# Optimization experiments

Measured on AMD Instinct MI355X. Metric: run time of the kernel, lower is better.

Reference implementation:

```python
import jax, jax.numpy as jnp
import numpy as np

D_MODEL, N_HEADS, D_STATE, N_GROUPS, CHUNK = 2048, 32, 64, 1, 256
BATCH, SEQLEN = 2, 4096


def setup_inputs() -> dict:
    key = jax.random.key(0)
    ks = jax.random.split(key, 8)
    s = 0.02
    d, h, n, g = D_MODEL, N_HEADS, D_STATE, N_GROUPS
    return {
        "x": jax.random.normal(ks[0], (BATCH, SEQLEN, d), jnp.float32),
        "A_log": jnp.log(jnp.arange(1, h + 1, dtype=jnp.float32)),
        "D": jnp.ones((h,), jnp.float32),
        "B_w": jax.random.normal(ks[1], (g * n, d), jnp.float32) * s,
        "B_b": jnp.zeros((g * n,), jnp.float32),
        "C_w": jax.random.normal(ks[2], (g * n, d), jnp.float32) * s,
        "C_b": jnp.zeros((g * n,), jnp.float32),
        "dt_w": jax.random.normal(ks[3], (h, d), jnp.float32) * s,
        "dt_b": jnp.zeros((h,), jnp.float32),
        "out_w": jax.random.normal(ks[4], (d, d), jnp.float32) * s,
        "out_b": jnp.zeros((d,), jnp.float32),
    }


def segsum(v):
    # v: [..., T] -> [..., T, T]; out[i,j] = sum_{k=j+1..i} v[k] for i>=j, -inf else
    cs = jnp.cumsum(v, axis=-1)
    seg = cs[..., :, None] - cs[..., None, :]
    T = v.shape[-1]
    mask = jnp.tril(jnp.ones((T, T), bool))
    return jnp.where(mask, seg, -jnp.inf)


def _ssd(x, A_log, D, B_w, B_b, C_w, C_b, dt_w, dt_b, out_w, out_b):
    b, t, d = x.shape
    h = A_log.shape[0]
    n = B_w.shape[0] // N_GROUPS
    p = d // h
    l = CHUNK
    c = t // l

    A = -jnp.exp(A_log.astype(jnp.float32))                      # [h]
    B = (x @ B_w.T + B_b).reshape(b, t, N_GROUPS, n)             # g=1
    C = (x @ C_w.T + C_b).reshape(b, t, N_GROUPS, n)
    B = jnp.broadcast_to(B, (b, t, h, n))                        # repeat groups -> heads
    C = jnp.broadcast_to(C, (b, t, h, n))
    dt = jax.nn.softplus(x @ dt_w.T + dt_b)                      # [b,t,h]
    xh = x.reshape(b, t, h, p)

    # chunked SSD (Mamba2 mamba_chunk_scan_combined math)
    xc = xh.reshape(b, c, l, h, p)
    Bc = B.reshape(b, c, l, h, n)
    Cc = C.reshape(b, c, l, h, n)
    dtc = dt.reshape(b, c, l, h)
    dA = jnp.transpose(dtc * A, (0, 3, 1, 2))                    # [b,h,c,l]
    A_cumsum = jnp.cumsum(dA, axis=-1)                           # [b,h,c,l]

    # 1. intra-chunk (diagonal blocks)
    L = jnp.exp(segsum(dA))                                      # [b,h,c,l,l]
    xdt = xc * dtc[..., None]                                    # [b,c,l,h,p]
    Y_diag = jnp.einsum('bclhn,bcshn,bhcls,bcshp->bclhp', Cc, Bc, L, xdt)

    # 2. per-chunk final states
    decay_states = jnp.exp(A_cumsum[..., -1:] - A_cumsum)        # [b,h,c,l]
    states = jnp.einsum('bclhn,bhcl,bclhp->bchpn', Bc, decay_states, xdt)

    # 3. inter-chunk recurrence on chunk states
    states = jnp.concatenate([jnp.zeros_like(states[:, :1]), states], axis=1)  # [b,c+1,h,p,n]
    dA_last = jnp.pad(A_cumsum[..., -1], ((0, 0), (0, 0), (1, 0)))             # [b,h,c+1]
    decay_chunk = jnp.exp(segsum(dA_last))                                     # [b,h,c+1,c+1]
    new_states = jnp.einsum('bhzc,bchpn->bzhpn', decay_chunk, states)
    prev_states = new_states[:, :-1]                                           # [b,c,h,p,n]

    # 4. state -> output contribution
    state_decay_out = jnp.exp(A_cumsum)                          # [b,h,c,l]
    Y_off = jnp.einsum('bclhn,bchpn,bhcl->bclhp', Cc, prev_states, state_decay_out)

    Y = (Y_diag + Y_off).reshape(b, t, h, p) + D[None, None, :, None] * xh
    return Y.reshape(b, t, d) @ out_w.T + out_b


def reference(x, A_log, D, B_w, B_b, C_w, C_b, dt_w, dt_b, out_w, out_b):
    return _ssd(x, A_log, D, B_w, B_b, C_w, C_b, dt_w, dt_b, out_w, out_b)
```

## Files before the change

### kernel.cpp

```cpp
#include <hip/hip_runtime.h>
#include <hip/hip_bf16.h>
#include <math.h>

namespace {
constexpr int kDModel = 2048;
constexpr int kHeads  = 32;
constexpr int kState  = 64;
constexpr int kP      = 64;
constexpr int kChunk  = 256;
constexpr int kNChunk = 16;
constexpr int kBatch  = 2;
constexpr int kSeq    = 4096;
constexpr int kM      = kBatch * kSeq;
}

typedef __bf16 bf16_t;
typedef __attribute__((ext_vector_type(8))) __bf16 bf16x8;
typedef __attribute__((ext_vector_type(4))) __bf16 bf16x4;
typedef __attribute__((ext_vector_type(4))) float f32x4;

__device__ __forceinline__ void gload_lds16(const void* g, void* l) {
    __builtin_amdgcn_global_load_lds(
        (const __attribute__((address_space(1))) void*)g,
        (__attribute__((address_space(3))) void*)l,
        16, 0, 0);
}

__global__ __launch_bounds__(256)
void gemm_bcdt(const bf16_t* __restrict__ A, const bf16_t* __restrict__ W,
               const float* __restrict__ b0, const float* __restrict__ b1,
               const float* __restrict__ b2,
               bf16_t* __restrict__ o0h, bf16_t* __restrict__ o1h,
               float* __restrict__ o2f)
{
    constexpr int K = kDModel;
    __shared__ __bf16 AstS[64 * 32];
    __shared__ __bf16 WstS[128 * 32];
    const int tid  = threadIdx.x;
    const int lane = tid & 63;
    const int wave = tid >> 6;
    const int wm = (wave >> 1) * 32;
    const int wn = (wave & 1) * 64;
    const int l15 = lane & 15, quad = lane >> 4;
    const int m0 = blockIdx.y * 64;
    const int n0 = blockIdx.x * 128;
    const int u0 = tid, u1 = tid + 256;

    f32x4 acc[2][4];
    #pragma unroll
    for (int i = 0; i < 2; ++i)
        #pragma unroll
        for (int j = 0; j < 4; ++j)
            acc[i][j] = (f32x4){0.f, 0.f, 0.f, 0.f};

    for (int k0 = 0; k0 < K; k0 += 32) {
        gload_lds16(A + (size_t)(m0 + (tid >> 2)) * K + k0 + (tid & 3) * 8, AstS + tid * 8);
        gload_lds16(W + (size_t)(n0 + (u0 >> 2)) * K + k0 + (u0 & 3) * 8, WstS + u0 * 8);
        gload_lds16(W + (size_t)(n0 + (u1 >> 2)) * K + k0 + (u1 & 3) * 8, WstS + u1 * 8);
        __syncthreads();
        bf16x8 af[2], bfr[4];
        #pragma unroll
        for (int mi = 0; mi < 2; ++mi)
            af[mi] = *reinterpret_cast<const bf16x8*>(&AstS[(wm + mi * 16 + l15) * 32 + quad * 8]);
        #pragma unroll
        for (int ni = 0; ni < 4; ++ni)
            bfr[ni] = *reinterpret_cast<const bf16x8*>(&WstS[(wn + ni * 16 + l15) * 32 + quad * 8]);
        #pragma unroll
        for (int mi = 0; mi < 2; ++mi)
            #pragma unroll
            for (int ni = 0; ni < 4; ++ni)
                acc[mi][ni] = __builtin_amdgcn_mfma_f32_16x16x32_bf16(
                    af[mi], bfr[ni], acc[mi][ni], 0, 0, 0);
        __syncthreads();
    }

    #pragma unroll
    for (int mi = 0; mi < 2; ++mi) {
        #pragma unroll
        for (int reg = 0; reg < 4; ++reg) {
            const int r = m0 + wm + mi * 16 + quad * 4 + reg;
            #pragma unroll
            for (int ni = 0; ni < 4; ++ni) {
                const float v = acc[mi][ni][reg];
                const int n = n0 + wn + ni * 16 + l15;
                if (n < 64) {
                    o0h[(size_t)r * 64 + n] = (bf16_t)(v + b0[n]);
                } else if (n < 128) {
                    o1h[(size_t)r * 64 + (n - 64)] = (bf16_t)(v + b1[n - 64]);
                } else if (n < 160) {
                    float z = v + b2[n - 128];
                    o2f[(size_t)r * 32 + (n - 128)] = (z > 20.f) ? z : log1pf(expf(z));
                }
            }
        }
    }
}

__global__ __launch_bounds__(512, 2)
void gemm256_out(const bf16_t* __restrict__ Ap, const bf16_t* __restrict__ Bp,
                 const float* __restrict__ bias, float* __restrict__ C)
{
    constexpr int M = 8192, N = 2048, NT = 2048 / 32;
    __shared__ __bf16 Ab[3][4 * 256 * 8];
    __shared__ __bf16 Bb[3][4 * 256 * 8];
    const int tid  = threadIdx.x;
    const int lane = tid & 63;
    const int wave = tid >> 6;
    const int l15 = lane & 15, quad = lane >> 4;
    const int bid = blockIdx.x;
    const int mt = (bid & 7) * 4 + ((bid >> 3) & 3);
    const int nt = bid >> 5;
    const int m0 = mt * 256;
    const int n0 = nt * 256;
    const int wm = (wave >> 2) * 128;
    const int wn = (wave & 3) * 64;

    const int u0 = tid, u1 = tid + 512;
    auto stage = [&](int t2, int stb) {
        const int ks0 = t2 * 4;
        const bf16_t* As = Ap + ((size_t)ks0 * M + m0) * 8;
        const bf16_t* Bs = Bp + ((size_t)ks0 * N + n0) * 8;
        __bf16* Al = &Ab[stb][0];
        __bf16* Bl = &Bb[stb][0];
        gload_lds16(As + ((size_t)(u0 >> 8) * M + (u0 & 255)) * 8, Al + u0 * 8);
        gload_lds16(As + ((size_t)(u1 >> 8) * M + (u1 & 255)) * 8, Al + u1 * 8);
        gload_lds16(Bs + ((size_t)(u0 >> 8) * N + (u0 & 255)) * 8, Bl + u0 * 8);
        gload_lds16(Bs + ((size_t)(u1 >> 8) * N + (u1 & 255)) * 8, Bl + u1 * 8);
    };

    f32x4 acc[8][4];
    #pragma unroll
    for (int i = 0; i < 8; ++i)
        #pragma unroll
        for (int j = 0; j < 4; ++j)
            acc[i][j] = (f32x4){0.f, 0.f, 0.f, 0.f};

    stage(0, 0);
    stage(1, 1);
    asm volatile("s_waitcnt vmcnt(4)" ::: "memory");
    __builtin_amdgcn_s_barrier();

    int cur = 0;
    for (int t = 0; t < NT; ++t) {
        const __bf16* Ac = &Ab[cur][0];
        const __bf16* Bc = &Bb[cur][0];
        int stb = cur + 2; if (stb >= 3) stb -= 3;

        bf16x8 af[4], bfr[4];
        #pragma unroll
        for (int mi = 0; mi < 4; ++mi)
            af[mi] = *reinterpret_cast<const bf16x8*>(
                &Ac[(quad * 256 + wm + mi * 16 + l15) * 8]);
        #pragma unroll
        for (int nj = 0; nj < 4; ++nj)
            bfr[nj] = *reinterpret_cast<const bf16x8*>(
                &Bc[(quad * 256 + wn + nj * 16 + l15) * 8]);
        if (t < NT - 2) stage(t + 2, stb);
        __builtin_amdgcn_s_setprio(1);
        #pragma unroll
        for (int mi = 0; mi < 4; ++mi)
            #pragma unroll
            for (int nj = 0; nj < 4; ++nj)
                acc[mi][nj] = __builtin_amdgcn_mfma_f32_16x16x32_bf16(
                    af[mi], bfr[nj], acc[mi][nj], 0, 0, 0);
        __builtin_amdgcn_s_setprio(0);

        #pragma unroll
        for (int mi = 0; mi < 4; ++mi)
            af[mi] = *reinterpret_cast<const bf16x8*>(
                &Ac[(quad * 256 + wm + 64 + mi * 16 + l15) * 8]);
        __builtin_amdgcn_s_setprio(1);
        #pragma unroll
        for (int mi = 0; mi < 4; ++mi)
            #pragma unroll
            for (int nj = 0; nj < 4; ++nj)
                acc[4 + mi][nj] = __builtin_amdgcn_mfma_f32_16x16x32_bf16(
                    af[mi], bfr[nj], acc[4 + mi][nj], 0, 0, 0);
        __builtin_amdgcn_s_setprio(0);

        if (t < NT - 2) {
            asm volatile("s_waitcnt vmcnt(4)" ::: "memory");
        } else if (t < NT - 1) {
            asm volatile("s_waitcnt vmcnt(0)" ::: "memory");
        }
        if (t < NT - 1) __builtin_amdgcn_s_barrier();
        cur = cur + 1; if (cur == 3) cur = 0;
    }

    float bia[4];
    #pragma unroll
    for (int nj = 0; nj < 4; ++nj) bia[nj] = bias[n0 + wn + nj * 16 + l15];
    #pragma unroll
    for (int mi = 0; mi < 8; ++mi) {
        #pragma unroll
        for (int reg = 0; reg < 4; ++reg) {
            const int r = m0 + wm + mi * 16 + quad * 4 + reg;
            #pragma unroll
            for (int nj = 0; nj < 4; ++nj) {
                const int c = n0 + wn + nj * 16 + l15;
                C[(size_t)r * N + c] = acc[mi][nj][reg] + bia[nj];
            }
        }
    }
}

__global__ __launch_bounds__(256)
void cvt_bf16_kernel(const float* __restrict__ src, bf16_t* __restrict__ dst, int n)
{
    const int i = (blockIdx.x * 256 + threadIdx.x) * 4;
    if (i + 3 < n) {
        const float4 v = *reinterpret_cast<const float4*>(src + i);
        dst[i + 0] = (bf16_t)v.x;
        dst[i + 1] = (bf16_t)v.y;
        dst[i + 2] = (bf16_t)v.z;
        dst[i + 3] = (bf16_t)v.w;
    }
}

__global__ __launch_bounds__(256)
void pack_wob_kernel(const float* __restrict__ W, bf16_t* __restrict__ Wp)
{
    const int idx = blockIdx.x * 256 + threadIdx.x;
    const int n = idx >> 8, ks = idx & 255;
    const float4 v0 = *reinterpret_cast<const float4*>(W + (size_t)n * 2048 + ks * 8);
    const float4 v1 = *reinterpret_cast<const float4*>(W + (size_t)n * 2048 + ks * 8 + 4);
    bf16x8 o;
    o[0] = (__bf16)v0.x; o[1] = (__bf16)v0.y; o[2] = (__bf16)v0.z; o[3] = (__bf16)v0.w;
    o[4] = (__bf16)v1.x; o[5] = (__bf16)v1.y; o[6] = (__bf16)v1.z; o[7] = (__bf16)v1.w;
    *reinterpret_cast<bf16x8*>(Wp + ((size_t)ks * 2048 + n) * 8) = o;
}

__global__ __launch_bounds__(256)
void pack_w_kernel(const float* __restrict__ B_w, const float* __restrict__ C_w,
                   const float* __restrict__ dt_w, bf16_t* __restrict__ wcat)
{
    const int idx = blockIdx.x * 256 + threadIdx.x;
    const int r = idx >> 11, k = idx & 2047;
    float v = 0.f;
    if (r < 64)       v = B_w[r * 2048 + k];
    else if (r < 128) v = C_w[(r - 64) * 2048 + k];
    else if (r < 160) v = dt_w[(r - 128) * 2048 + k];
    wcat[idx] = (bf16_t)v;
}

__global__ __launch_bounds__(kChunk)
void dtcumsum_kernel(const float* __restrict__ dtm, const float* __restrict__ A_log,
                     float* __restrict__ Acs)
{
    const int blk = blockIdx.x;
    const int ci = blk & (kNChunk - 1);
    const int hi = (blk >> 4) & (kHeads - 1);
    const int bi = blk >> 9;
    const int t = threadIdx.x;
    const float Ah = -expf(A_log[hi]);
    __shared__ float s[kChunk];
    s[t] = dtm[((size_t)bi * kSeq + ci * kChunk + t) * kHeads + hi] * Ah;
    __syncthreads();
    for (int off = 1; off < kChunk; off <<= 1) {
        const float add = (t >= off) ? s[t - off] : 0.f;
        __syncthreads();
        s[t] += add;
        __syncthreads();
    }
    Acs[((size_t)(bi * kHeads + hi) * kNChunk + ci) * kChunk + t] = s[t];
}

__global__ __launch_bounds__(256)
void bT_kernel(const bf16_t* __restrict__ Bb16, bf16_t* __restrict__ bTg)
{
    const int ci = blockIdx.x & (kNChunk - 1);
    const int bi = blockIdx.x >> 4;
    const size_t rowbase = (size_t)bi * kSeq + ci * kChunk;
    __shared__ __bf16 T[64 * 264];
    const int tid = threadIdx.x;
    bf16x8 v[8];
    #pragma unroll
    for (int e = 0; e < 8; ++e)
        v[e] = *reinterpret_cast<const bf16x8*>(Bb16 + (rowbase + tid) * 64 + e * 8);
    #pragma unroll
    for (int e = 0; e < 8; ++e)
        #pragma unroll
        for (int j = 0; j < 8; ++j)
            T[(e * 8 + j) * 264 + tid] = v[e][j];
    __syncthreads();
    const int n = tid >> 2, seg = (tid & 3) * 64;
    bf16_t* dst = bTg + ((size_t)(bi * kNChunk + ci)) * (64 * 256) + n * 256 + seg;
    #pragma unroll
    for (int j = 0; j < 8; ++j) {
        *reinterpret_cast<bf16x8*>(dst + j * 8) =
            *reinterpret_cast<const bf16x8*>(&T[n * 264 + seg + j * 8]);
    }
}

__global__ __launch_bounds__(256)
void xdtT_kernel(const bf16_t* __restrict__ xb, const float* __restrict__ dtm,
                 bf16_t* __restrict__ xdtT)
{
    const int blk = blockIdx.x;
    const int hi = blk & (kHeads - 1);
    const int ci = (blk >> 5) & (kNChunk - 1);
    const int bi = blk >> 9;
    const size_t rowbase = (size_t)bi * kSeq + ci * kChunk;
    __shared__ __bf16 T[64 * 264];
    const int tid = threadIdx.x;
    const float d = dtm[(rowbase + tid) * kHeads + hi];
    bf16x8 v[8];
    #pragma unroll
    for (int e = 0; e < 8; ++e)
        v[e] = *reinterpret_cast<const bf16x8*>(xb + (rowbase + tid) * kDModel + hi * kP + e * 8);
    #pragma unroll
    for (int e = 0; e < 8; ++e)
        #pragma unroll
        for (int j = 0; j < 8; ++j)
            T[(e * 8 + j) * 264 + tid] = (__bf16)((float)v[e][j] * d);
    __syncthreads();
    const int p = tid >> 2, seg = (tid & 3) * 64;
    bf16_t* dst = xdtT + (size_t)blk * (64 * 256) + p * 256 + seg;
    #pragma unroll
    for (int j = 0; j < 8; ++j) {
        *reinterpret_cast<bf16x8*>(dst + j * 8) =
            *reinterpret_cast<const bf16x8*>(&T[p * 264 + seg + j * 8]);
    }
}

__global__ __launch_bounds__(256)
void states_mfma(const bf16_t* __restrict__ xdtT, const bf16_t* __restrict__ bTg,
                 const float* __restrict__ Acs, float* __restrict__ states)
{
    const int blk = blockIdx.x;
    const int hi = blk & (kHeads - 1);
    const int ci = (blk >> 5) & (kNChunk - 1);
    const int bi = blk >> 9;
    __shared__ __bf16 Xa[64 * 264];
    __shared__ __bf16 Bt[64 * 264];
    __shared__ float dec[kChunk];
    const int tid = threadIdx.x;
    const int lane = tid & 63;
    const int wave = tid >> 6;
    const int l15 = lane & 15, quad = lane >> 4;

    const float* acs = Acs + ((size_t)(bi * kHeads + hi) * kNChunk + ci) * kChunk;
    dec[tid] = expf(acs[kChunk - 1] - acs[tid]);
    __syncthreads();

    const bf16_t* bsrc = bTg + ((size_t)(bi * kNChunk + ci)) * (64 * 256);
    const bf16_t* xsrc = xdtT + (size_t)blk * (64 * 256);
    #pragma unroll
    for (int e = 0; e < 8; ++e) {
        const int u = e * 256 + tid;
        const int r = u >> 5, seg = (u & 31) * 8;
        *reinterpret_cast<bf16x8*>(&Bt[r * 264 + seg]) =
            *reinterpret_cast<const bf16x8*>(bsrc + r * 256 + seg);
        bf16x8 xv = *reinterpret_cast<const bf16x8*>(xsrc + r * 256 + seg);
        bf16x8 xo;
        #pragma unroll
        for (int j = 0; j < 8; ++j)
            xo[j] = (__bf16)((float)xv[j] * dec[seg + j]);
        *reinterpret_cast<bf16x8*>(&Xa[r * 264 + seg]) = xo;
    }
    __syncthreads();

    f32x4 acc[4];
    #pragma unroll
    for (int ni = 0; ni < 4; ++ni) acc[ni] = (f32x4){0.f, 0.f, 0.f, 0.f};
    #pragma unroll
    for (int kk = 0; kk < 8; ++kk) {
        const bf16x8 af = *reinterpret_cast<const bf16x8*>(
            &Xa[(wave * 16 + l15) * 264 + kk * 32 + quad * 8]);
        #pragma unroll
        for (int ni = 0; ni < 4; ++ni) {
            const bf16x8 bf = *reinterpret_cast<const bf16x8*>(
                &Bt[(ni * 16 + l15) * 264 + kk * 32 + quad * 8]);
            acc[ni] = __builtin_amdgcn_mfma_f32_16x16x32_bf16(af, bf, acc[ni], 0, 0, 0);
        }
    }
    float* sp = states + (size_t)blk * (kP * kState);
    #pragma unroll
    for (int reg = 0; reg < 4; ++reg) {
        const int p = wave * 16 + quad * 4 + reg;
        #pragma unroll
        for (int ni = 0; ni < 4; ++ni)
            sp[(size_t)p * kState + ni * 16 + l15] = acc[ni][reg];
    }
}

__global__ __launch_bounds__(256)
void chunkscan_kernel(const float* __restrict__ states, const float* __restrict__ Acs,
                      float* __restrict__ prevs)
{
    const int q  = blockIdx.x & 15;
    const int hi = (blockIdx.x >> 4) & (kHeads - 1);
    const int bi = blockIdx.x >> 9;
    const int e  = q * 256 + threadIdx.x;
    __shared__ float ea[kNChunk];
    if (threadIdx.x < kNChunk)
        ea[threadIdx.x] = expf(Acs[((size_t)(bi * kHeads + hi) * kNChunk + threadIdx.x)
                                   * kChunk + kChunk - 1]);
    __syncthreads();
    float P = 0.f;
    prevs[((size_t)(bi * kNChunk + 0) * kHeads + hi) * (kP * kState) + e] = 0.f;
    for (int c = 1; c < kNChunk; ++c) {
        P = fmaf(ea[c - 1], P,
                 states[((size_t)(bi * kNChunk + (c - 1)) * kHeads + hi) * (kP * kState) + e]);
        prevs[((size_t)(bi * kNChunk + c) * kHeads + hi) * (kP * kState) + e] = P;
    }
}

__global__ __launch_bounds__(256)
void ychunk_mfma(const float* __restrict__ x, const bf16_t* __restrict__ Bb16,
                 const bf16_t* __restrict__ Cb16, const bf16_t* __restrict__ xdtT,
                 const float* __restrict__ Acs, const float* __restrict__ prevs,
                 const float* __restrict__ Dvec, bf16_t* __restrict__ Yp)
{
    const int blk = blockIdx.x;
    const int lt = blk & 3;
    const int hi = (blk >> 2) & (kHeads - 1);
    const int ci = (blk >> 7) & (kNChunk - 1);
    const int bi = blk >> 11;
    __shared__ float acs_s[kChunk];
    __shared__ __bf16 Cs[64 * 72];
    __shared__ __bf16 Bs[64 * 72];
    __shared__ __bf16 Xt[64 * 72];
    __shared__ __bf16 Sp[64 * 72];
    const int tid = threadIdx.x;
    const int lane = tid & 63;
    const int wave = tid >> 6;
    const int l15 = lane & 15, quad = lane >> 4;
    const size_t rowbase = (size_t)bi * kSeq + ci * kChunk;
    const bf16_t* xdsrc = xdtT + ((size_t)((bi * kNChunk + ci) * kHeads + hi)) * (64 * 256);

    acs_s[tid] = Acs[((size_t)(bi * kHeads + hi) * kNChunk + ci) * kChunk + tid];
    #pragma unroll
    for (int e = 0; e < 2; ++e) {
        const int u = e * 256 + tid;
        const int r = u >> 3, seg = (u & 7) * 8;
        *reinterpret_cast<bf16x8*>(&Cs[r * 72 + seg]) =
            *reinterpret_cast<const bf16x8*>(Cb16 + (rowbase + lt * 64 + r) * 64 + seg);
    }
    const float* pp = prevs + ((size_t)(bi * kNChunk + ci) * kHeads + hi) * (kP * kState);
    #pragma unroll
    for (int e = 0; e < 4; ++e) {
        const int idx = e * 1024 + tid * 4;
        const int r = idx >> 6, c = idx & 63;
        const float4 vp = *reinterpret_cast<const float4*>(pp + idx);
        bf16x4 p4;
        p4[0] = (__bf16)vp.x; p4[1] = (__bf16)vp.y;
        p4[2] = (__bf16)vp.z; p4[3] = (__bf16)vp.w;
        *reinterpret_cast<bf16x4*>(&Bs[r * 72 + c]) = p4;
    }
    __syncthreads();

    bf16x8 af[2];
    af[0] = *reinterpret_cast<const bf16x8*>(&Cs[(wave * 16 + l15) * 72 + quad * 8]);
    af[1] = *reinterpret_cast<const bf16x8*>(&Cs[(wave * 16 + l15) * 72 + 32 + quad * 8]);

    f32x4 yacc[4];
    #pragma unroll
    for (int ni = 0; ni < 4; ++ni) yacc[ni] = (f32x4){0.f, 0.f, 0.f, 0.f};
    #pragma unroll
    for (int ni = 0; ni < 4; ++ni) {
        const bf16x8 b0 = *reinterpret_cast<const bf16x8*>(&Bs[(ni * 16 + l15) * 72 + quad * 8]);
        const bf16x8 b1 = *reinterpret_cast<const bf16x8*>(&Bs[(ni * 16 + l15) * 72 + 32 + quad * 8]);
        yacc[ni] = __builtin_amdgcn_mfma_f32_16x16x32_bf16(af[0], b0, yacc[ni], 0, 0, 0);
        yacc[ni] = __builtin_amdgcn_mfma_f32_16x16x32_bf16(af[1], b1, yacc[ni], 0, 0, 0);
    }
    const int mrow = wave * 16 + quad * 4;
    {
        float es[4];
        #pragma unroll
        for (int reg = 0; reg < 4; ++reg) es[reg] = expf(acs_s[lt * 64 + mrow + reg]);
        #pragma unroll
        for (int ni = 0; ni < 4; ++ni)
            #pragma unroll
            for (int reg = 0; reg < 4; ++reg) yacc[ni][reg] *= es[reg];
    }

    for (int st = 0; st <= lt; ++st) {
        __syncthreads();
        #pragma unroll
        for (int e = 0; e < 2; ++e) {
            const int u = e * 256 + tid;
            const int r = u >> 3, seg = (u & 7) * 8;
            *reinterpret_cast<bf16x8*>(&Bs[r * 72 + seg]) =
                *reinterpret_cast<const bf16x8*>(Bb16 + (rowbase + st * 64 + r) * 64 + seg);
            *reinterpret_cast<bf16x8*>(&Xt[r * 72 + seg]) =
                *reinterpret_cast<const bf16x8*>(xdsrc + r * 256 + st * 64 + seg);
        }
        __syncthreads();
        f32x4 sacc[4];
        #pragma unroll
        for (int ni = 0; ni < 4; ++ni) sacc[ni] = (f32x4){0.f, 0.f, 0.f, 0.f};
        #pragma unroll
        for (int ni = 0; ni < 4; ++ni) {
            const bf16x8 b0 = *reinterpret_cast<const bf16x8*>(&Bs[(ni * 16 + l15) * 72 + quad * 8]);
            const bf16x8 b1 = *reinterpret_cast<const bf16x8*>(&Bs[(ni * 16 + l15) * 72 + 32 + quad * 8]);
            sacc[ni] = __builtin_amdgcn_mfma_f32_16x16x32_bf16(af[0], b0, sacc[ni], 0, 0, 0);
            sacc[ni] = __builtin_amdgcn_mfma_f32_16x16x32_bf16(af[1], b1, sacc[ni], 0, 0, 0);
        }
        #pragma unroll
        for (int reg = 0; reg < 4; ++reg) {
            const int l = lt * 64 + mrow + reg;
            const float al = acs_s[l];
            #pragma unroll
            for (int ni = 0; ni < 4; ++ni) {
                const int scol = ni * 16 + l15;
                const int sg = st * 64 + scol;
                float v = sacc[ni][reg] * expf(al - acs_s[sg]);
                if (st == lt && sg > l) v = 0.f;
                Sp[(mrow + reg) * 72 + scol] = (__bf16)v;
            }
        }
        __syncthreads();
        const bf16x8 as0 = *reinterpret_cast<const bf16x8*>(&Sp[(wave * 16 + l15) * 72 + quad * 8]);
        const bf16x8 as1 = *reinterpret_cast<const bf16x8*>(&Sp[(wave * 16 + l15) * 72 + 32 + quad * 8]);
        #pragma unroll
        for (int ni = 0; ni < 4; ++ni) {
            const bf16x8 x0 = *reinterpret_cast<const bf16x8*>(&Xt[(ni * 16 + l15) * 72 + quad * 8]);
            const bf16x8 x1 = *reinterpret_cast<const bf16x8*>(&Xt[(ni * 16 + l15) * 72 + 32 + quad * 8]);
            yacc[ni] = __builtin_amdgcn_mfma_f32_16x16x32_bf16(as0, x0, yacc[ni], 0, 0, 0);
            yacc[ni] = __builtin_amdgcn_mfma_f32_16x16x32_bf16(as1, x1, yacc[ni], 0, 0, 0);
        }
    }

    const float Dh = Dvec[hi];
    #pragma unroll
    for (int reg = 0; reg < 4; ++reg) {
        const size_t tg = rowbase + lt * 64 + mrow + reg;
        #pragma unroll
        for (int ni = 0; ni < 4; ++ni) {
            const int p = ni * 16 + l15;
            const float v = yacc[ni][reg] + Dh * x[tg * kDModel + hi * kP + p];
            Yp[((size_t)(hi * 8 + (p >> 3)) * (size_t)kM + tg) * 8 + (p & 7)] = (bf16_t)v;
        }
    }
}

extern "C" void kernel_launch(void* const* d_in, const int* in_sizes, int n_in,
                              void* d_out, int out_size, void* d_ws, size_t ws_size,
                              hipStream_t stream)
{
    (void)in_sizes; (void)n_in; (void)out_size; (void)ws_size;
    const float* x     = (const float*)d_in[0];
    const float* A_log = (const float*)d_in[1];
    const float* Dvec  = (const float*)d_in[2];
    const float* B_w   = (const float*)d_in[3];
    const float* B_b   = (const float*)d_in[4];
    const float* C_w   = (const float*)d_in[5];
    const float* C_b   = (const float*)d_in[6];
    const float* dt_w  = (const float*)d_in[7];
    const float* dt_b  = (const float*)d_in[8];
    const float* out_w = (const float*)d_in[9];
    const float* out_b = (const float*)d_in[10];
    float* out = (float*)d_out;

    float* ws = (float*)d_ws;
    float* dtm    = ws;
    float* Acs    = dtm + (size_t)kM * kHeads;
    float* states = Acs + (size_t)kBatch * kHeads * kNChunk * kChunk;
    float* prevs  = states + (size_t)kBatch * kNChunk * kHeads * kP * kState;
    bf16_t* xb    = (bf16_t*)(prevs + (size_t)kBatch * kNChunk * kHeads * kP * kState);
    bf16_t* Y     = xb;
    bf16_t* Bb16  = xb + (size_t)kM * kDModel;
    bf16_t* Cb16  = Bb16 + (size_t)kM * kState;
    bf16_t* xdtT  = Cb16 + (size_t)kM * kState;
    bf16_t* bTg   = xdtT + (size_t)kM * kDModel;
    bf16_t* wcat  = bTg + (size_t)kBatch * kNChunk * kState * kChunk;
    bf16_t* wob   = wcat + (size_t)256 * kDModel;

    const dim3 blk(256);
    cvt_bf16_kernel<<<dim3(kM * kDModel / 1024), blk, 0, stream>>>(x, xb, kM * kDModel);
    pack_wob_kernel<<<dim3(kDModel * 256 / 256), blk, 0, stream>>>(out_w, wob);
    pack_w_kernel<<<dim3(256 * kDModel / 256), blk, 0, stream>>>(B_w, C_w, dt_w, wcat);
    gemm_bcdt<<<dim3(2, kM / 64), blk, 0, stream>>>(xb, wcat,
                                                    B_b, C_b, dt_b,
                                                    Bb16, Cb16, dtm);
    dtcumsum_kernel<<<dim3(kBatch * kHeads * kNChunk), dim3(kChunk), 0, stream>>>(dtm, A_log, Acs);
    bT_kernel<<<dim3(kBatch * kNChunk), blk, 0, stream>>>(Bb16, bTg);
    xdtT_kernel<<<dim3(kBatch * kNChunk * kHeads), blk, 0, stream>>>(xb, dtm, xdtT);
    states_mfma<<<dim3(kBatch * kNChunk * kHeads), blk, 0, stream>>>(xdtT, bTg, Acs, states);
    chunkscan_kernel<<<dim3(kBatch * kHeads * 16), blk, 0, stream>>>(states, Acs, prevs);
    ychunk_mfma<<<dim3(kBatch * kNChunk * kHeads * 4), blk, 0, stream>>>(
        x, Bb16, Cb16, xdtT, Acs, prevs, Dvec, Y);
    gemm256_out<<<dim3(256), dim3(512), 0, stream>>>(Y, wob, out_b, out);
}
```

Before: 351.9 us.

## Fuse prep kernels, store prev states in bf16, derive skip term from staged xdt

Merges the three fp32-to-bf16 conversion and packing kernels into one launch that dispatches by block index. The chunk scan now writes the previous states directly in bf16, which halves that traffic and removes the conversion inside ychunk. ychunk stops rereading fp32 x for the D skip term and instead recovers x from the xdt tile already in shared memory, dividing by dt. A __syncthreads before reading Sp becomes a waitcnt plus sched_barrier. The division adds bf16 rounding error and breaks if dt is near zero. The relaxed barrier assumes each wave reads back only the Sp rows it wrote itself.

```diff
diff --git a/kernel.cpp b/kernel.cpp
--- a/kernel.cpp
+++ b/kernel.cpp
@@ -205,42 +205,37 @@
 }
 
 __global__ __launch_bounds__(256)
-void cvt_bf16_kernel(const float* __restrict__ src, bf16_t* __restrict__ dst, int n)
-{
-    const int i = (blockIdx.x * 256 + threadIdx.x) * 4;
-    if (i + 3 < n) {
-        const float4 v = *reinterpret_cast<const float4*>(src + i);
-        dst[i + 0] = (bf16_t)v.x;
-        dst[i + 1] = (bf16_t)v.y;
-        dst[i + 2] = (bf16_t)v.z;
-        dst[i + 3] = (bf16_t)v.w;
-    }
-}
-
-__global__ __launch_bounds__(256)
-void pack_wob_kernel(const float* __restrict__ W, bf16_t* __restrict__ Wp)
-{
-    const int idx = blockIdx.x * 256 + threadIdx.x;
-    const int n = idx >> 8, ks = idx & 255;
-    const float4 v0 = *reinterpret_cast<const float4*>(W + (size_t)n * 2048 + ks * 8);
-    const float4 v1 = *reinterpret_cast<const float4*>(W + (size_t)n * 2048 + ks * 8 + 4);
-    bf16x8 o;
-    o[0] = (__bf16)v0.x; o[1] = (__bf16)v0.y; o[2] = (__bf16)v0.z; o[3] = (__bf16)v0.w;
-    o[4] = (__bf16)v1.x; o[5] = (__bf16)v1.y; o[6] = (__bf16)v1.z; o[7] = (__bf16)v1.w;
-    *reinterpret_cast<bf16x8*>(Wp + ((size_t)ks * 2048 + n) * 8) = o;
-}
-
-__global__ __launch_bounds__(256)
-void pack_w_kernel(const float* __restrict__ B_w, const float* __restrict__ C_w,
-                   const float* __restrict__ dt_w, bf16_t* __restrict__ wcat)
-{
-    const int idx = blockIdx.x * 256 + threadIdx.x;
-    const int r = idx >> 11, k = idx & 2047;
-    float v = 0.f;
-    if (r < 64)       v = B_w[r * 2048 + k];
-    else if (r < 128) v = C_w[(r - 64) * 2048 + k];
-    else if (r < 160) v = dt_w[(r - 128) * 2048 + k];
-    wcat[idx] = (bf16_t)v;
+void prep_fused(const float* __restrict__ x, bf16_t* __restrict__ xb,
+                const float* __restrict__ W, bf16_t* __restrict__ Wp,
+                const float* __restrict__ B_w, const float* __restrict__ C_w,
+                const float* __restrict__ dt_w, bf16_t* __restrict__ wcat)
+{
+    const int bid = blockIdx.x;
+    if (bid < 16384) {
+        const int i = (bid * 256 + threadIdx.x) * 4;
+        const float4 v = *reinterpret_cast<const float4*>(x + i);
+        xb[i + 0] = (bf16_t)v.x;
+        xb[i + 1] = (bf16_t)v.y;
+        xb[i + 2] = (bf16_t)v.z;
+        xb[i + 3] = (bf16_t)v.w;
+    } else if (bid < 16384 + 2048) {
+        const int idx = (bid - 16384) * 256 + threadIdx.x;
+        const int n = idx >> 8, ks = idx & 255;
+        const float4 v0 = *reinterpret_cast<const float4*>(W + (size_t)n * 2048 + ks * 8);
+        const float4 v1 = *reinterpret_cast<const float4*>(W + (size_t)n * 2048 + ks * 8 + 4);
+        bf16x8 o;
+        o[0] = (__bf16)v0.x; o[1] = (__bf16)v0.y; o[2] = (__bf16)v0.z; o[3] = (__bf16)v0.w;
+        o[4] = (__bf16)v1.x; o[5] = (__bf16)v1.y; o[6] = (__bf16)v1.z; o[7] = (__bf16)v1.w;
+        *reinterpret_cast<bf16x8*>(Wp + ((size_t)ks * 2048 + n) * 8) = o;
+    } else {
+        const int idx = (bid - 16384 - 2048) * 256 + threadIdx.x;
+        const int r = idx >> 11, k = idx & 2047;
+        float v = 0.f;
+        if (r < 64)       v = B_w[r * 2048 + k];
+        else if (r < 128) v = C_w[(r - 64) * 2048 + k];
+        else if (r < 160) v = dt_w[(r - 128) * 2048 + k];
+        wcat[idx] = (bf16_t)v;
+    }
 }
 
 __global__ __launch_bounds__(kChunk)
@@ -386,7 +381,7 @@
 
 __global__ __launch_bounds__(256)
 void chunkscan_kernel(const float* __restrict__ states, const float* __restrict__ Acs,
-                      float* __restrict__ prevs)
+                      bf16_t* __restrict__ prevsb)
 {
     const int q  = blockIdx.x & 15;
     const int hi = (blockIdx.x >> 4) & (kHeads - 1);
@@ -398,18 +393,18 @@
                                    * kChunk + kChunk - 1]);
     __syncthreads();
     float P = 0.f;
-    prevs[((size_t)(bi * kNChunk + 0) * kHeads + hi) * (kP * kState) + e] = 0.f;
+    prevsb[((size_t)(bi * kNChunk + 0) * kHeads + hi) * (kP * kState) + e] = (bf16_t)0.f;
     for (int c = 1; c < kNChunk; ++c) {
         P = fmaf(ea[c - 1], P,
                  states[((size_t)(bi * kNChunk + (c - 1)) * kHeads + hi) * (kP * kState) + e]);
-        prevs[((size_t)(bi * kNChunk + c) * kHeads + hi) * (kP * kState) + e] = P;
-    }
-}
-
-__global__ __launch_bounds__(256)
-void ychunk_mfma(const float* __restrict__ x, const bf16_t* __restrict__ Bb16,
-                 const bf16_t* __restrict__ Cb16, const bf16_t* __restrict__ xdtT,
-                 const float* __restrict__ Acs, const float* __restrict__ prevs,
+        prevsb[((size_t)(bi * kNChunk + c) * kHeads + hi) * (kP * kState) + e] = (bf16_t)P;
+    }
+}
+
+__global__ __launch_bounds__(256)
+void ychunk_mfma(const bf16_t* __restrict__ Bb16, const bf16_t* __restrict__ Cb16,
+                 const bf16_t* __restrict__ xdtT, const float* __restrict__ Acs,
+                 const bf16_t* __restrict__ prevsb, const float* __restrict__ dtm,
                  const float* __restrict__ Dvec, bf16_t* __restrict__ Yp)
 {
     const int blk = blockIdx.x;
@@ -418,6 +413,7 @@
     const int ci = (blk >> 7) & (kNChunk - 1);
     const int bi = blk >> 11;
     __shared__ float acs_s[kChunk];
+    __shared__ float dts_s[64];
     __shared__ __bf16 Cs[64 * 72];
     __shared__ __bf16 Bs[64 * 72];
     __shared__ __bf16 Xt[64 * 72];
@@ -426,27 +422,21 @@
     const int lane = tid & 63;
     const int wave = tid >> 6;
     const int l15 = lane & 15, quad = lane >> 4;
+    const int mrow = wave * 16 + quad * 4;
     const size_t rowbase = (size_t)bi * kSeq + ci * kChunk;
     const bf16_t* xdsrc = xdtT + ((size_t)((bi * kNChunk + ci) * kHeads + hi)) * (64 * 256);
 
     acs_s[tid] = Acs[((size_t)(bi * kHeads + hi) * kNChunk + ci) * kChunk + tid];
+    if (tid < 64) dts_s[tid] = dtm[(rowbase + lt * 64 + tid) * kHeads + hi];
+    const bf16_t* pp = prevsb + ((size_t)(bi * kNChunk + ci) * kHeads + hi) * (kP * kState);
     #pragma unroll
     for (int e = 0; e < 2; ++e) {
         const int u = e * 256 + tid;
         const int r = u >> 3, seg = (u & 7) * 8;
         *reinterpret_cast<bf16x8*>(&Cs[r * 72 + seg]) =
             *reinterpret_cast<const bf16x8*>(Cb16 + (rowbase + lt * 64 + r) * 64 + seg);
-    }
-    const float* pp = prevs + ((size_t)(bi * kNChunk + ci) * kHeads + hi) * (kP * kState);
-    #pragma unroll
-    for (int e = 0; e < 4; ++e) {
-        const int idx = e * 1024 + tid * 4;
-        const int r = idx >> 6, c = idx & 63;
-        const float4 vp = *reinterpret_cast<const float4*>(pp + idx);
-        bf16x4 p4;
-        p4[0] = (__bf16)vp.x; p4[1] = (__bf16)vp.y;
-        p4[2] = (__bf16)vp.z; p4[3] = (__bf16)vp.w;
-        *reinterpret_cast<bf16x4*>(&Bs[r * 72 + c]) = p4;
+        *reinterpret_cast<bf16x8*>(&Bs[r * 72 + seg]) =
+            *reinterpret_cast<const bf16x8*>(pp + r * 64 + seg);
     }
     __syncthreads();
 
@@ -464,7 +454,6 @@
         yacc[ni] = __builtin_amdgcn_mfma_f32_16x16x32_bf16(af[0], b0, yacc[ni], 0, 0, 0);
         yacc[ni] = __builtin_amdgcn_mfma_f32_16x16x32_bf16(af[1], b1, yacc[ni], 0, 0, 0);
     }
-    const int mrow = wave * 16 + quad * 4;
     {
         float es[4];
         #pragma unroll
@@ -510,7 +499,8 @@
                 Sp[(mrow + reg) * 72 + scol] = (__bf16)v;
             }
         }
-        __syncthreads();
+        asm volatile("s_waitcnt lgkmcnt(0)" ::: "memory");
+        __builtin_amdgcn_sched_barrier(0);
         const bf16x8 as0 = *reinterpret_cast<const bf16x8*>(&Sp[(wave * 16 + l15) * 72 + quad * 8]);
         const bf16x8 as1 = *reinterpret_cast<const bf16x8*>(&Sp[(wave * 16 + l15) * 72 + 32 + quad * 8]);
         #pragma unroll
@@ -525,11 +515,14 @@
     const float Dh = Dvec[hi];
     #pragma unroll
     for (int reg = 0; reg < 4; ++reg) {
-        const size_t tg = rowbase + lt * 64 + mrow + reg;
+        const int lrow = mrow + reg;
+        const size_t tg = rowbase + lt * 64 + lrow;
+        const float dinv = 1.f / dts_s[lrow];
         #pragma unroll
         for (int ni = 0; ni < 4; ++ni) {
             const int p = ni * 16 + l15;
-            const float v = yacc[ni][reg] + Dh * x[tg * kDModel + hi * kP + p];
+            const float xv = (float)Xt[p * 72 + lrow] * dinv;
+            const float v = yacc[ni][reg] + Dh * xv;
             Yp[((size_t)(hi * 8 + (p >> 3)) * (size_t)kM + tg) * 8 + (p & 7)] = (bf16_t)v;
         }
     }
@@ -557,8 +550,8 @@
     float* dtm    = ws;
     float* Acs    = dtm + (size_t)kM * kHeads;
     float* states = Acs + (size_t)kBatch * kHeads * kNChunk * kChunk;
-    float* prevs  = states + (size_t)kBatch * kNChunk * kHeads * kP * kState;
-    bf16_t* xb    = (bf16_t*)(prevs + (size_t)kBatch * kNChunk * kHeads * kP * kState);
+    bf16_t* prevsb = (bf16_t*)(states + (size_t)kBatch * kNChunk * kHeads * kP * kState);
+    bf16_t* xb    = prevsb + (size_t)kBatch * kNChunk * kHeads * kP * kState;
     bf16_t* Y     = xb;
     bf16_t* Bb16  = xb + (size_t)kM * kDModel;
     bf16_t* Cb16  = Bb16 + (size_t)kM * kState;
@@ -568,18 +561,16 @@
     bf16_t* wob   = wcat + (size_t)256 * kDModel;
 
     const dim3 blk(256);
-    cvt_bf16_kernel<<<dim3(kM * kDModel / 1024), blk, 0, stream>>>(x, xb, kM * kDModel);
-    pack_wob_kernel<<<dim3(kDModel * 256 / 256), blk, 0, stream>>>(out_w, wob);
-    pack_w_kernel<<<dim3(256 * kDModel / 256), blk, 0, stream>>>(B_w, C_w, dt_w, wcat);
-    gemm_bcdt<<<dim3(2, kM / 64), blk, 0, stream>>>(xb, wcat,
-                                                    B_b, C_b, dt_b,
+    prep_fused<<<dim3(16384 + 2048 + 2048), blk, 0, stream>>>(
+        x, xb, out_w, wob, B_w, C_w, dt_w, wcat);
+    gemm_bcdt<<<dim3(2, kM / 64), blk, 0, stream>>>(xb, wcat, B_b, C_b, dt_b,
                                                     Bb16, Cb16, dtm);
     dtcumsum_kernel<<<dim3(kBatch * kHeads * kNChunk), dim3(kChunk), 0, stream>>>(dtm, A_log, Acs);
     bT_kernel<<<dim3(kBatch * kNChunk), blk, 0, stream>>>(Bb16, bTg);
     xdtT_kernel<<<dim3(kBatch * kNChunk * kHeads), blk, 0, stream>>>(xb, dtm, xdtT);
     states_mfma<<<dim3(kBatch * kNChunk * kHeads), blk, 0, stream>>>(xdtT, bTg, Acs, states);
-    chunkscan_kernel<<<dim3(kBatch * kHeads * 16), blk, 0, stream>>>(states, Acs, prevs);
+    chunkscan_kernel<<<dim3(kBatch * kHeads * 16), blk, 0, stream>>>(states, Acs, prevsb);
     ychunk_mfma<<<dim3(kBatch * kNChunk * kHeads * 4), blk, 0, stream>>>(
-        x, Bb16, Cb16, xdtT, Acs, prevs, Dvec, Y);
+        Bb16, Cb16, xdtT, Acs, prevsb, dtm, Dvec, Y);
     gemm256_out<<<dim3(256), dim3(512), 0, stream>>>(Y, wob, out_b, out);
 }
```

Measured after the change: 353.3 us. No clear change (+0.4%).
